# Kernel tuning notes

Measured on AMD Instinct MI355X. Metric: run time of the kernel, lower is better.

## Reference

```python
import jax, jax.numpy as jnp
import numpy as np

N = 50000
E = 800000
IN_C = 128
HID = 128
OUT_C = 2


def _linear_params(key, fan_in, fan_out):
    k1, k2 = jax.random.split(key)
    bound = 1.0 / np.sqrt(fan_in)
    W = jax.random.uniform(k1, (fan_in, fan_out), jnp.float32, -bound, bound)
    b = jax.random.uniform(k2, (fan_out,), jnp.float32, -bound, bound)
    return W, b


def setup_inputs() -> dict:
    key = jax.random.key(0)
    ks = jax.random.split(key, 9)
    x = jax.random.normal(ks[0], (N, IN_C), jnp.float32)
    edge_index = jax.random.randint(ks[1], (2, E), 0, N, jnp.int64)
    W1a, b1a = _linear_params(ks[2], IN_C, HID)
    W1b, b1b = _linear_params(ks[3], HID, HID)
    W2a, b2a = _linear_params(ks[4], HID, HID)
    W2b, b2b = _linear_params(ks[5], HID, HID)
    Wfc, bfc = _linear_params(ks[6], HID, OUT_C)
    return {
        "x": x, "edge_index": edge_index,
        "W1a": W1a, "b1a": b1a, "W1b": W1b, "b1b": b1b,
        "W2a": W2a, "b2a": b2a, "W2b": W2b, "b2b": b2b,
        "Wfc": Wfc, "bfc": bfc,
    }


def _gin_conv(x, src, dst, Wa, ba, Wb, bb):
    # GINConv with eps=0: h = MLP(x + sum_{j in N(i)} x_j)
    agg = jax.ops.segment_sum(x[src], dst, num_segments=N)  # [N, d]
    h = x + agg
    h = jax.nn.relu(h @ Wa + ba)
    return h @ Wb + bb


def reference(x, edge_index, W1a, b1a, W1b, b1b, W2a, b2a, W2b, b2b, Wfc, bfc):
    src, dst = edge_index[0], edge_index[1]  # messages flow src -> dst
    h = _gin_conv(x, src, dst, W1a, b1a, W1b, b1b)
    h = jax.nn.relu(h)
    # dropout is identity in eval mode
    h = _gin_conv(h, src, dst, W2a, b2a, W2b, b2b)
    return h @ Wfc + bfc  # [N, 2]
```

## Files before the change

### kernel.cpp

```cpp
#include <hip/hip_runtime.h>

#define N_NODES 50000
#define N_EDGES 800000
#define NBUK    392
#define B_BIN   128
#define EPB     6250
#define NCVT    1024
#define CAPB    2560

typedef unsigned short u16;
typedef unsigned int   u32;
typedef __bf16 bf16x8 __attribute__((ext_vector_type(8)));
typedef float  f32x4  __attribute__((ext_vector_type(4)));

__device__ __forceinline__ float bf_lo(u32 v){ return __uint_as_float(v << 16); }
__device__ __forceinline__ float bf_hi(u32 v){ return __uint_as_float(v & 0xffff0000u); }
__device__ __forceinline__ u32 bf_pack(float a, float b){
    u32 ua = __float_as_uint(a), ub = __float_as_uint(b);
    ua += 0x7fffu + ((ua >> 16) & 1u);
    ub += 0x7fffu + ((ub >> 16) & 1u);
    return (ua >> 16) | (ub & 0xffff0000u);
}
__device__ __forceinline__ u16 f2bf(float a){
    u32 ua = __float_as_uint(a);
    ua += 0x7fffu + ((ua >> 16) & 1u);
    return (u16)(ua >> 16);
}
__device__ __forceinline__ void addu4(uint4 v, float* a){
    a[0] += bf_lo(v.x); a[1] += bf_hi(v.x);
    a[2] += bf_lo(v.y); a[3] += bf_hi(v.y);
    a[4] += bf_lo(v.z); a[5] += bf_hi(v.z);
    a[6] += bf_lo(v.w); a[7] += bf_hi(v.w);
}

__device__ __forceinline__ int blockScan256(int v, int* ws, int t) {
    int lane = t & 63, w = t >> 6;
    #pragma unroll
    for (int off = 1; off < 64; off <<= 1) {
        int u = __shfl_up(v, off);
        if (lane >= off) v += u;
    }
    if (lane == 63) ws[w] = v;
    __syncthreads();
    int add = 0;
    for (int k = 0; k < w; k++) add += ws[k];
    return v + add;
}

__device__ __forceinline__ int blockScan512(int v, int* ws, int t) {
    int lane = t & 63, w = t >> 6;
    #pragma unroll
    for (int off = 1; off < 64; off <<= 1) {
        int u = __shfl_up(v, off);
        if (lane >= off) v += u;
    }
    if (lane == 63) ws[w] = v;
    __syncthreads();
    int add = 0;
    for (int k = 0; k < w; k++) add += ws[k];
    return v + add;
}

__launch_bounds__(256)
__global__ void binA_kernel(const int* __restrict__ esrc, const int* __restrict__ edst,
                            u32* __restrict__ bukBuf, int* __restrict__ bukCnt,
                            const float* __restrict__ xsrc, u32* __restrict__ xb,
                            const float* __restrict__ W1a, const float* __restrict__ W1b,
                            const float* __restrict__ W2a, const float* __restrict__ W2b,
                            const float* __restrict__ Wfc, const float* __restrict__ b2b,
                            const float* __restrict__ bfc,
                            u16* __restrict__ wt1a, u16* __restrict__ wt1b,
                            u16* __restrict__ wt2a,
                            float* __restrict__ Wc, float* __restrict__ bc) {
    int t = threadIdx.x, blk = blockIdx.x;
    __shared__ u32 ebuf[EPB];
    __shared__ int hist[NBUK];
    __shared__ int cur[NBUK];
    __shared__ int gbase[NBUK];
    __shared__ int ws[4];
    if (blk >= B_BIN) {
        int pb = blk - B_BIN;
        if (pb < 192) {
            int g  = pb * 256 + t;
            int mi = g >> 14;
            int p  = g & 16383;
            int k  = p >> 7, m = p & 127;
            const float* src = (mi == 0) ? W1a : (mi == 1) ? W1b : W2a;
            u16* dst         = (mi == 0) ? wt1a : (mi == 1) ? wt1b : wt2a;
            dst[m * 128 + k] = f2bf(src[k * 128 + m]);
            return;
        }
        if (pb == 192) {
            int j = t >> 1, o = t & 1;
            float s = 0.f;
            for (int k = 0; k < 128; k++)
                s += W2b[j * 128 + k] * Wfc[k * 2 + o];
            Wc[j * 2 + o] = s;
            if (t < 2) {
                float s2 = 0.f;
                for (int k = 0; k < 128; k++)
                    s2 += b2b[k] * Wfc[k * 2 + t];
                bc[t] = s2 + bfc[t];
            }
            return;
        }
        int cb = pb - 193;
        const int total = N_NODES * 64;
        for (int i = cb * 256 + t; i < total; i += NCVT * 256) {
            float2 f = ((const float2*)xsrc)[i];
            xb[i] = bf_pack(f.x, f.y);
        }
        return;
    }
    int base = blk * EPB;
    for (int i = t; i < NBUK; i += 256) hist[i] = 0;
    __syncthreads();
    for (int i = t; i < EPB; i += 256)
        atomicAdd(&hist[edst[base + i] >> 7], 1);
    __syncthreads();
    int c0 = 0, c1 = 0;
    if (t < 196) { c0 = hist[2 * t]; c1 = hist[2 * t + 1]; }
    int s2 = c0 + c1;
    int incl = blockScan256(s2, ws, t);
    int excl = incl - s2;
    if (t < 196) {
        hist[2 * t]     = excl;          cur[2 * t]     = excl;
        hist[2 * t + 1] = excl + c0;     cur[2 * t + 1] = excl + c0;
    }
    __syncthreads();
    for (int i = t; i < EPB; i += 256) {
        int gi = base + i;
        int d = edst[gi], s = esrc[gi];
        u32 e = (u32)s | ((u32)(d & 127) << 16) | ((u32)(d >> 7) << 23);
        int p = atomicAdd(&cur[d >> 7], 1);
        ebuf[p] = e;
    }
    __syncthreads();
    for (int j = t; j < NBUK; j += 256) {
        int cnt = cur[j] - hist[j];
        gbase[j] = cnt ? atomicAdd(&bukCnt[j], cnt) : 0;
    }
    __syncthreads();
    for (int i = t; i < EPB; i += 256) {
        u32 e = ebuf[i];
        int b9 = (int)(e >> 23);
        u32 idx = (u32)(gbase[b9] + (i - hist[b9]));
        if (idx < CAPB)
            bukBuf[(size_t)b9 * CAPB + idx] = e;
    }
}

__launch_bounds__(512, 4)
__global__ void bconv1_kernel(const u32* __restrict__ bukBuf,
                              const int* __restrict__ bukCnt,
                              const u32* __restrict__ xb,
                              const u16* __restrict__ WA, const float* __restrict__ bA,
                              const u16* __restrict__ WB, const float* __restrict__ bB,
                              int2* __restrict__ span, int* __restrict__ csr,
                              u16* __restrict__ h1, int n) {
    __shared__ __align__(16) char shbuf[34816 + 10240 + 512 + 512 + 32 + 16];
    u16 (*As)[136] = (u16(*)[136])shbuf;
    u32* ebuf      = (u32*)shbuf;
    int* cbuf      = (int*)(shbuf + 34816);
    int* hist      = (int*)(shbuf + 34816 + 10240);
    int* cursor    = (int*)(shbuf + 34816 + 10240 + 512);
    int* ws        = (int*)(shbuf + 34816 + 10240 + 1024);
    int b = blockIdx.x, t = threadIdx.x;

    int tot = bukCnt[b];
    if (tot > CAPB) tot = CAPB;
    if (t < 128) hist[t] = 0;
    __syncthreads();
    for (int i = t; i < tot; i += 512) {
        u32 e = bukBuf[(size_t)b * CAPB + i];
        ebuf[i] = e;
        atomicAdd(&hist[(e >> 16) & 127], 1);
    }
    __syncthreads();
    int hv = (t < 128) ? hist[t] : 0;
    int hincl = blockScan512(hv, ws, t);
    int hexcl = hincl - hv;
    int gb = b * CAPB;
    if (t < 128) {
        hist[t]   = hexcl;
        cursor[t] = hexcl;
        int node = (b << 7) + t;
        if (node < n) span[node] = make_int2(gb + hexcl, gb + hexcl + hv);
    }
    __syncthreads();
    for (int i = t; i < tot; i += 512) {
        u32 e = ebuf[i];
        int p = atomicAdd(&cursor[(e >> 16) & 127], 1);
        cbuf[p] = (int)(e & 0xFFFFu);
    }
    __syncthreads();
    for (int i = t; i < tot; i += 512)
        csr[gb + i] = cbuf[i];
    __syncthreads();

    int row0 = b * 128;
    int w = t >> 6, lane = t & 63;
    int g4 = lane >> 4, l16 = lane & 15;
    const uint4* xp = (const uint4*)xb;
    #pragma unroll
    for (int p = 0; p < 4; p++) {
        int rl = w * 16 + p * 4 + g4;
        int node = row0 + rl;
        float a[8] = {0.f,0.f,0.f,0.f,0.f,0.f,0.f,0.f};
        if (node < n) {
            addu4(xp[(size_t)node * 16 + l16], a);
            int j = hist[rl], jend = cursor[rl];
            for (; j + 8 <= jend; j += 8) {
                int s0 = cbuf[j],     s1 = cbuf[j + 1], s2b = cbuf[j + 2], s3 = cbuf[j + 3];
                int s4 = cbuf[j + 4], s5 = cbuf[j + 5], s6 = cbuf[j + 6], s7 = cbuf[j + 7];
                uint4 v0 = xp[(size_t)s0 * 16 + l16], v1 = xp[(size_t)s1 * 16 + l16];
                uint4 v2 = xp[(size_t)s2b * 16 + l16], v3 = xp[(size_t)s3 * 16 + l16];
                uint4 v4 = xp[(size_t)s4 * 16 + l16], v5 = xp[(size_t)s5 * 16 + l16];
                uint4 v6 = xp[(size_t)s6 * 16 + l16], v7 = xp[(size_t)s7 * 16 + l16];
                addu4(v0, a); addu4(v1, a); addu4(v2, a); addu4(v3, a);
                addu4(v4, a); addu4(v5, a); addu4(v6, a); addu4(v7, a);
            }
            for (; j + 4 <= jend; j += 4) {
                int s0 = cbuf[j], s1 = cbuf[j + 1], s2b = cbuf[j + 2], s3 = cbuf[j + 3];
                uint4 v0 = xp[(size_t)s0 * 16 + l16], v1 = xp[(size_t)s1 * 16 + l16];
                uint4 v2 = xp[(size_t)s2b * 16 + l16], v3 = xp[(size_t)s3 * 16 + l16];
                addu4(v0, a); addu4(v1, a); addu4(v2, a); addu4(v3, a);
            }
            for (; j < jend; j++)
                addu4(xp[(size_t)cbuf[j] * 16 + l16], a);
        }
        uint4 pk = make_uint4(bf_pack(a[0], a[1]), bf_pack(a[2], a[3]),
                              bf_pack(a[4], a[5]), bf_pack(a[6], a[7]));
        *(uint4*)&As[rl][l16 * 8] = pk;
    }
    int lm = l16, lq = g4;
    f32x4 acc[8];
    #pragma unroll
    for (int c = 0; c < 8; c++) acc[c] = (f32x4){0.f, 0.f, 0.f, 0.f};
    #pragma unroll
    for (int kk = 0; kk < 4; kk++) {
        bf16x8 af = *(const bf16x8*)&As[w * 16 + lm][kk * 32 + lq * 8];
        #pragma unroll
        for (int c = 0; c < 8; c++) {
            bf16x8 bf = *(const bf16x8*)(WA + (size_t)(c * 16 + lm) * 128 + kk * 32 + lq * 8);
            acc[c] = __builtin_amdgcn_mfma_f32_16x16x32_bf16(af, bf, acc[c], 0, 0, 0);
        }
    }
    #pragma unroll
    for (int c = 0; c < 8; c++) {
        int col = c * 16 + lm;
        float bcol = bA[col];
        #pragma unroll
        for (int r = 0; r < 4; r++) {
            float v = acc[c][r] + bcol;
            v = v > 0.f ? v : 0.f;
            As[w * 16 + lq * 4 + r][col] = f2bf(v);
        }
    }
    f32x4 acc2[8];
    #pragma unroll
    for (int c = 0; c < 8; c++) acc2[c] = (f32x4){0.f, 0.f, 0.f, 0.f};
    #pragma unroll
    for (int kk = 0; kk < 4; kk++) {
        bf16x8 af = *(const bf16x8*)&As[w * 16 + lm][kk * 32 + lq * 8];
        #pragma unroll
        for (int c = 0; c < 8; c++) {
            bf16x8 bf = *(const bf16x8*)(WB + (size_t)(c * 16 + lm) * 128 + kk * 32 + lq * 8);
            acc2[c] = __builtin_amdgcn_mfma_f32_16x16x32_bf16(af, bf, acc2[c], 0, 0, 0);
        }
    }
    #pragma unroll
    for (int c = 0; c < 8; c++) {
        int col = c * 16 + lm;
        float bcol = bB[col];
        #pragma unroll
        for (int r = 0; r < 4; r++) {
            int row = row0 + w * 16 + lq * 4 + r;
            if (row < n) {
                float v = acc2[c][r] + bcol;
                v = v > 0.f ? v : 0.f;
                h1[(size_t)row * 128 + col] = f2bf(v);
            }
        }
    }
}

__launch_bounds__(256, 4)
__global__ void fconv2_kernel(const u32* __restrict__ xb,
                              const u16* __restrict__ WA, const float* __restrict__ bA,
                              const float* __restrict__ Wc, const float* __restrict__ bc,
                              const int2* __restrict__ span, const int* __restrict__ csr,
                              float2* __restrict__ out, int n) {
    __shared__ u16 As[64][136];
    int t = threadIdx.x;
    int row0 = blockIdx.x * 64;
    int w = t >> 6, lane = t & 63;
    int g4 = lane >> 4, l16 = lane & 15;
    const uint4* xp = (const uint4*)xb;
    #pragma unroll
    for (int p = 0; p < 4; p++) {
        int rl = w * 16 + p * 4 + g4;
        int node = row0 + rl;
        float a[8] = {0.f,0.f,0.f,0.f,0.f,0.f,0.f,0.f};
        if (node < n) {
            addu4(xp[(size_t)node * 16 + l16], a);
            int2 sp = span[node];
            int j = sp.x, jend = sp.y;
            for (; j + 8 <= jend; j += 8) {
                int s0 = csr[j],     s1 = csr[j + 1], s2 = csr[j + 2], s3 = csr[j + 3];
                int s4 = csr[j + 4], s5 = csr[j + 5], s6 = csr[j + 6], s7 = csr[j + 7];
                uint4 v0 = xp[(size_t)s0 * 16 + l16], v1 = xp[(size_t)s1 * 16 + l16];
                uint4 v2 = xp[(size_t)s2 * 16 + l16], v3 = xp[(size_t)s3 * 16 + l16];
                uint4 v4 = xp[(size_t)s4 * 16 + l16], v5 = xp[(size_t)s5 * 16 + l16];
                uint4 v6 = xp[(size_t)s6 * 16 + l16], v7 = xp[(size_t)s7 * 16 + l16];
                addu4(v0, a); addu4(v1, a); addu4(v2, a); addu4(v3, a);
                addu4(v4, a); addu4(v5, a); addu4(v6, a); addu4(v7, a);
            }
            for (; j + 4 <= jend; j += 4) {
                int s0 = csr[j], s1 = csr[j + 1], s2 = csr[j + 2], s3 = csr[j + 3];
                uint4 v0 = xp[(size_t)s0 * 16 + l16], v1 = xp[(size_t)s1 * 16 + l16];
                uint4 v2 = xp[(size_t)s2 * 16 + l16], v3 = xp[(size_t)s3 * 16 + l16];
                addu4(v0, a); addu4(v1, a); addu4(v2, a); addu4(v3, a);
            }
            for (; j < jend; j++)
                addu4(xp[(size_t)csr[j] * 16 + l16], a);
        }
        uint4 pk = make_uint4(bf_pack(a[0], a[1]), bf_pack(a[2], a[3]),
                              bf_pack(a[4], a[5]), bf_pack(a[6], a[7]));
        *(uint4*)&As[rl][l16 * 8] = pk;
    }
    int lm = l16, lq = g4;
    f32x4 acc[8];
    #pragma unroll
    for (int c = 0; c < 8; c++) acc[c] = (f32x4){0.f, 0.f, 0.f, 0.f};
    #pragma unroll
    for (int kk = 0; kk < 4; kk++) {
        bf16x8 af = *(const bf16x8*)&As[w * 16 + lm][kk * 32 + lq * 8];
        #pragma unroll
        for (int c = 0; c < 8; c++) {
            bf16x8 bf = *(const bf16x8*)(WA + (size_t)(c * 16 + lm) * 128 + kk * 32 + lq * 8);
            acc[c] = __builtin_amdgcn_mfma_f32_16x16x32_bf16(af, bf, acc[c], 0, 0, 0);
        }
    }
    float p0[4] = {0,0,0,0}, p1[4] = {0,0,0,0};
    #pragma unroll
    for (int c = 0; c < 8; c++) {
        int col = c * 16 + lm;
        float bcol = bA[col];
        float2 wc = ((const float2*)Wc)[col];
        #pragma unroll
        for (int r = 0; r < 4; r++) {
            float v = acc[c][r] + bcol;
            v = v > 0.f ? v : 0.f;
            p0[r] += v * wc.x;
            p1[r] += v * wc.y;
        }
    }
    #pragma unroll
    for (int off = 1; off < 16; off <<= 1) {
        #pragma unroll
        for (int r = 0; r < 4; r++) {
            p0[r] += __shfl_xor(p0[r], off);
            p1[r] += __shfl_xor(p1[r], off);
        }
    }
    if (lm == 0) {
        float b0 = bc[0], b1 = bc[1];
        #pragma unroll
        for (int r = 0; r < 4; r++) {
            int row = row0 + w * 16 + lq * 4 + r;
            if (row < n) out[row] = make_float2(p0[r] + b0, p1[r] + b1);
        }
    }
}

extern "C" void kernel_launch(void* const* d_in, const int* in_sizes, int n_in,
                              void* d_out, int out_size, void* d_ws, size_t ws_size,
                              hipStream_t stream) {
    const float* x   = (const float*)d_in[0];
    const int*   ei  = (const int*)d_in[1];
    const float* W1a = (const float*)d_in[2];
    const float* b1a = (const float*)d_in[3];
    const float* W1b = (const float*)d_in[4];
    const float* b1b = (const float*)d_in[5];
    const float* W2a = (const float*)d_in[6];
    const float* b2a = (const float*)d_in[7];
    const float* W2b = (const float*)d_in[8];
    const float* b2b = (const float*)d_in[9];
    const float* Wfc = (const float*)d_in[10];
    const float* bfc = (const float*)d_in[11];

    const int* esrc = ei;
    const int* edst = ei + N_EDGES;

    char* w = (char*)d_ws;
    size_t off = 0;
    auto alloc = [&](size_t bytes) -> char* {
        char* p = w + off;
        off = (off + bytes + 255) & ~(size_t)255;
        return p;
    };
    int2*  span       = (int2*)alloc((size_t)N_NODES * 8);
    int*   csr        = (int*)alloc((size_t)NBUK * CAPB * 4);
    u32*   bukBuf     = (u32*)alloc((size_t)NBUK * CAPB * 4);
    int*   bukCnt     = (int*)alloc((size_t)NBUK * 4);
    u16*   wt1a       = (u16*)alloc(128 * 128 * 2);
    u16*   wt1b       = (u16*)alloc(128 * 128 * 2);
    u16*   wt2a       = (u16*)alloc(128 * 128 * 2);
    float* Wc         = (float*)alloc(256 * 4);
    float* bc         = (float*)alloc(2 * 4);
    u16*   bufA       = (u16*)alloc((size_t)N_NODES * 128 * 2);
    u16*   bufB       = (u16*)alloc((size_t)N_NODES * 128 * 2);

    hipMemsetAsync(bukCnt, 0, (size_t)NBUK * 4, stream);
    binA_kernel<<<B_BIN + 193 + NCVT, 256, 0, stream>>>(esrc, edst, bukBuf, bukCnt,
                                                        x, (u32*)bufB,
                                                        W1a, W1b, W2a, W2b, Wfc, b2b, bfc,
                                                        wt1a, wt1b, wt2a, Wc, bc);
    bconv1_kernel<<<NBUK, 512, 0, stream>>>(bukBuf, bukCnt,
                                            (const u32*)bufB, wt1a, b1a, wt1b, b1b,
                                            span, csr, bufA, N_NODES);
    fconv2_kernel<<<(N_NODES + 63) / 64, 256, 0, stream>>>((const u32*)bufA, wt2a, b2a,
                                                           Wc, bc, span, csr,
                                                           (float2*)d_out, N_NODES);
}
```

Measured before the change: 213.0 us.

## Split CSR build from conv1 and use persistent per-wave tile queues

Moves CSR construction out of the fused conv1 kernel into its own kernel. Both convolution kernels become persistent grids in which each wave independently takes 16-row tiles, first from a static per-block chunk and then from a global atomic counter. The aim is to even out the load imbalance caused by varying node degrees, which previously left whole 128-row blocks waiting at barriers. The cost is an extra kernel launch, a reread of csr from global memory instead of LDS in conv1, and atomic contention on the tile counters.

```diff
diff --git a/kernel.cpp b/kernel.cpp
--- a/kernel.cpp
+++ b/kernel.cpp
@@ -7,6 +7,10 @@
 #define EPB     6250
 #define NCVT    1024
 #define CAPB    2560
+#define NTILES  3125
+#define CGRID   768
+#define SCHUNK  3
+#define QBASE   (CGRID*SCHUNK)
 
 typedef unsigned short u16;
 typedef unsigned int   u32;
@@ -150,23 +154,15 @@
     }
 }
 
-__launch_bounds__(512, 4)
-__global__ void bconv1_kernel(const u32* __restrict__ bukBuf,
-                              const int* __restrict__ bukCnt,
-                              const u32* __restrict__ xb,
-                              const u16* __restrict__ WA, const float* __restrict__ bA,
-                              const u16* __restrict__ WB, const float* __restrict__ bB,
-                              int2* __restrict__ span, int* __restrict__ csr,
-                              u16* __restrict__ h1, int n) {
-    __shared__ __align__(16) char shbuf[34816 + 10240 + 512 + 512 + 32 + 16];
-    u16 (*As)[136] = (u16(*)[136])shbuf;
-    u32* ebuf      = (u32*)shbuf;
-    int* cbuf      = (int*)(shbuf + 34816);
-    int* hist      = (int*)(shbuf + 34816 + 10240);
-    int* cursor    = (int*)(shbuf + 34816 + 10240 + 512);
-    int* ws        = (int*)(shbuf + 34816 + 10240 + 1024);
+__launch_bounds__(512)
+__global__ void csrb_kernel(const u32* __restrict__ bukBuf, const int* __restrict__ bukCnt,
+                            int2* __restrict__ span, int* __restrict__ csr, int n) {
+    __shared__ u32 ebuf[CAPB];
+    __shared__ int cbuf[CAPB];
+    __shared__ int hist[128];
+    __shared__ int cursor[128];
+    __shared__ int ws[8];
     int b = blockIdx.x, t = threadIdx.x;
-
     int tot = bukCnt[b];
     if (tot > CAPB) tot = CAPB;
     if (t < 128) hist[t] = 0;
@@ -196,113 +192,37 @@
     __syncthreads();
     for (int i = t; i < tot; i += 512)
         csr[gb + i] = cbuf[i];
-    __syncthreads();
-
-    int row0 = b * 128;
+}
+
+__launch_bounds__(512, 4)
+__global__ void conv1q_kernel(const u32* __restrict__ xb,
+                              const u16* __restrict__ WA, const float* __restrict__ bA,
+                              const u16* __restrict__ WB, const float* __restrict__ bB,
+                              const int2* __restrict__ span, const int* __restrict__ csr,
+                              u16* __restrict__ h1, int* __restrict__ gctr) {
+    __shared__ __align__(16) u16 As[128][136];
+    __shared__ int lqc;
+    int t = threadIdx.x;
+    if (t == 0) lqc = 0;
+    __syncthreads();
     int w = t >> 6, lane = t & 63;
     int g4 = lane >> 4, l16 = lane & 15;
     const uint4* xp = (const uint4*)xb;
-    #pragma unroll
-    for (int p = 0; p < 4; p++) {
-        int rl = w * 16 + p * 4 + g4;
-        int node = row0 + rl;
-        float a[8] = {0.f,0.f,0.f,0.f,0.f,0.f,0.f,0.f};
-        if (node < n) {
-            addu4(xp[(size_t)node * 16 + l16], a);
-            int j = hist[rl], jend = cursor[rl];
-            for (; j + 8 <= jend; j += 8) {
-                int s0 = cbuf[j],     s1 = cbuf[j + 1], s2b = cbuf[j + 2], s3 = cbuf[j + 3];
-                int s4 = cbuf[j + 4], s5 = cbuf[j + 5], s6 = cbuf[j + 6], s7 = cbuf[j + 7];
-                uint4 v0 = xp[(size_t)s0 * 16 + l16], v1 = xp[(size_t)s1 * 16 + l16];
-                uint4 v2 = xp[(size_t)s2b * 16 + l16], v3 = xp[(size_t)s3 * 16 + l16];
-                uint4 v4 = xp[(size_t)s4 * 16 + l16], v5 = xp[(size_t)s5 * 16 + l16];
-                uint4 v6 = xp[(size_t)s6 * 16 + l16], v7 = xp[(size_t)s7 * 16 + l16];
-                addu4(v0, a); addu4(v1, a); addu4(v2, a); addu4(v3, a);
-                addu4(v4, a); addu4(v5, a); addu4(v6, a); addu4(v7, a);
-            }
-            for (; j + 4 <= jend; j += 4) {
-                int s0 = cbuf[j], s1 = cbuf[j + 1], s2b = cbuf[j + 2], s3 = cbuf[j + 3];
-                uint4 v0 = xp[(size_t)s0 * 16 + l16], v1 = xp[(size_t)s1 * 16 + l16];
-                uint4 v2 = xp[(size_t)s2b * 16 + l16], v3 = xp[(size_t)s3 * 16 + l16];
-                addu4(v0, a); addu4(v1, a); addu4(v2, a); addu4(v3, a);
-            }
-            for (; j < jend; j++)
-                addu4(xp[(size_t)cbuf[j] * 16 + l16], a);
-        }
-        uint4 pk = make_uint4(bf_pack(a[0], a[1]), bf_pack(a[2], a[3]),
-                              bf_pack(a[4], a[5]), bf_pack(a[6], a[7]));
-        *(uint4*)&As[rl][l16 * 8] = pk;
-    }
-    int lm = l16, lq = g4;
-    f32x4 acc[8];
-    #pragma unroll
-    for (int c = 0; c < 8; c++) acc[c] = (f32x4){0.f, 0.f, 0.f, 0.f};
-    #pragma unroll
-    for (int kk = 0; kk < 4; kk++) {
-        bf16x8 af = *(const bf16x8*)&As[w * 16 + lm][kk * 32 + lq * 8];
-        #pragma unroll
-        for (int c = 0; c < 8; c++) {
-            bf16x8 bf = *(const bf16x8*)(WA + (size_t)(c * 16 + lm) * 128 + kk * 32 + lq * 8);
-            acc[c] = __builtin_amdgcn_mfma_f32_16x16x32_bf16(af, bf, acc[c], 0, 0, 0);
-        }
-    }
-    #pragma unroll
-    for (int c = 0; c < 8; c++) {
-        int col = c * 16 + lm;
-        float bcol = bA[col];
-        #pragma unroll
-        for (int r = 0; r < 4; r++) {
-            float v = acc[c][r] + bcol;
-            v = v > 0.f ? v : 0.f;
-            As[w * 16 + lq * 4 + r][col] = f2bf(v);
-        }
-    }
-    f32x4 acc2[8];
-    #pragma unroll
-    for (int c = 0; c < 8; c++) acc2[c] = (f32x4){0.f, 0.f, 0.f, 0.f};
-    #pragma unroll
-    for (int kk = 0; kk < 4; kk++) {
-        bf16x8 af = *(const bf16x8*)&As[w * 16 + lm][kk * 32 + lq * 8];
-        #pragma unroll
-        for (int c = 0; c < 8; c++) {
-            bf16x8 bf = *(const bf16x8*)(WB + (size_t)(c * 16 + lm) * 128 + kk * 32 + lq * 8);
-            acc2[c] = __builtin_amdgcn_mfma_f32_16x16x32_bf16(af, bf, acc2[c], 0, 0, 0);
-        }
-    }
-    #pragma unroll
-    for (int c = 0; c < 8; c++) {
-        int col = c * 16 + lm;
-        float bcol = bB[col];
-        #pragma unroll
-        for (int r = 0; r < 4; r++) {
-            int row = row0 + w * 16 + lq * 4 + r;
-            if (row < n) {
-                float v = acc2[c][r] + bcol;
-                v = v > 0.f ? v : 0.f;
-                h1[(size_t)row * 128 + col] = f2bf(v);
-            }
-        }
-    }
-}
-
-__launch_bounds__(256, 4)
-__global__ void fconv2_kernel(const u32* __restrict__ xb,
-                              const u16* __restrict__ WA, const float* __restrict__ bA,
-                              const float* __restrict__ Wc, const float* __restrict__ bc,
-                              const int2* __restrict__ span, const int* __restrict__ csr,
-                              float2* __restrict__ out, int n) {
-    __shared__ u16 As[64][136];
-    int t = threadIdx.x;
-    int row0 = blockIdx.x * 64;
-    int w = t >> 6, lane = t & 63;
-    int g4 = lane >> 4, l16 = lane & 15;
-    const uint4* xp = (const uint4*)xb;
-    #pragma unroll
-    for (int p = 0; p < 4; p++) {
-        int rl = w * 16 + p * 4 + g4;
-        int node = row0 + rl;
-        float a[8] = {0.f,0.f,0.f,0.f,0.f,0.f,0.f,0.f};
-        if (node < n) {
+    int sbase = blockIdx.x * SCHUNK;
+    for (;;) {
+        int tk;
+        if (lane == 0) {
+            tk = atomicAdd(&lqc, 1);
+            tk = (tk < SCHUNK) ? (sbase + tk) : (QBASE + atomicAdd(gctr, 1));
+        }
+        tk = __shfl(tk, 0);
+        if (tk >= NTILES) break;
+        int row0 = tk << 4;
+        #pragma unroll
+        for (int p = 0; p < 4; p++) {
+            int rl = p * 4 + g4;
+            int node = row0 + rl;
+            float a[8] = {0.f,0.f,0.f,0.f,0.f,0.f,0.f,0.f};
             addu4(xp[(size_t)node * 16 + l16], a);
             int2 sp = span[node];
             int j = sp.x, jend = sp.y;
@@ -324,52 +244,155 @@
             }
             for (; j < jend; j++)
                 addu4(xp[(size_t)csr[j] * 16 + l16], a);
-        }
-        uint4 pk = make_uint4(bf_pack(a[0], a[1]), bf_pack(a[2], a[3]),
-                              bf_pack(a[4], a[5]), bf_pack(a[6], a[7]));
-        *(uint4*)&As[rl][l16 * 8] = pk;
-    }
-    int lm = l16, lq = g4;
-    f32x4 acc[8];
-    #pragma unroll
-    for (int c = 0; c < 8; c++) acc[c] = (f32x4){0.f, 0.f, 0.f, 0.f};
-    #pragma unroll
-    for (int kk = 0; kk < 4; kk++) {
-        bf16x8 af = *(const bf16x8*)&As[w * 16 + lm][kk * 32 + lq * 8];
+            uint4 pk = make_uint4(bf_pack(a[0], a[1]), bf_pack(a[2], a[3]),
+                                  bf_pack(a[4], a[5]), bf_pack(a[6], a[7]));
+            *(uint4*)&As[w * 16 + rl][l16 * 8] = pk;
+        }
+        f32x4 acc[8];
+        #pragma unroll
+        for (int c = 0; c < 8; c++) acc[c] = (f32x4){0.f, 0.f, 0.f, 0.f};
+        #pragma unroll
+        for (int kk = 0; kk < 4; kk++) {
+            bf16x8 af = *(const bf16x8*)&As[w * 16 + l16][kk * 32 + g4 * 8];
+            #pragma unroll
+            for (int c = 0; c < 8; c++) {
+                bf16x8 bf = *(const bf16x8*)(WA + (size_t)(c * 16 + l16) * 128 + kk * 32 + g4 * 8);
+                acc[c] = __builtin_amdgcn_mfma_f32_16x16x32_bf16(af, bf, acc[c], 0, 0, 0);
+            }
+        }
         #pragma unroll
         for (int c = 0; c < 8; c++) {
-            bf16x8 bf = *(const bf16x8*)(WA + (size_t)(c * 16 + lm) * 128 + kk * 32 + lq * 8);
-            acc[c] = __builtin_amdgcn_mfma_f32_16x16x32_bf16(af, bf, acc[c], 0, 0, 0);
-        }
-    }
-    float p0[4] = {0,0,0,0}, p1[4] = {0,0,0,0};
-    #pragma unroll
-    for (int c = 0; c < 8; c++) {
-        int col = c * 16 + lm;
-        float bcol = bA[col];
-        float2 wc = ((const float2*)Wc)[col];
-        #pragma unroll
-        for (int r = 0; r < 4; r++) {
-            float v = acc[c][r] + bcol;
-            v = v > 0.f ? v : 0.f;
-            p0[r] += v * wc.x;
-            p1[r] += v * wc.y;
-        }
-    }
-    #pragma unroll
-    for (int off = 1; off < 16; off <<= 1) {
-        #pragma unroll
-        for (int r = 0; r < 4; r++) {
-            p0[r] += __shfl_xor(p0[r], off);
-            p1[r] += __shfl_xor(p1[r], off);
-        }
-    }
-    if (lm == 0) {
-        float b0 = bc[0], b1 = bc[1];
-        #pragma unroll
-        for (int r = 0; r < 4; r++) {
-            int row = row0 + w * 16 + lq * 4 + r;
-            if (row < n) out[row] = make_float2(p0[r] + b0, p1[r] + b1);
+            int col = c * 16 + l16;
+            float bcol = bA[col];
+            #pragma unroll
+            for (int r = 0; r < 4; r++) {
+                float v = acc[c][r] + bcol;
+                v = v > 0.f ? v : 0.f;
+                As[w * 16 + g4 * 4 + r][col] = f2bf(v);
+            }
+        }
+        f32x4 acc2[8];
+        #pragma unroll
+        for (int c = 0; c < 8; c++) acc2[c] = (f32x4){0.f, 0.f, 0.f, 0.f};
+        #pragma unroll
+        for (int kk = 0; kk < 4; kk++) {
+            bf16x8 af = *(const bf16x8*)&As[w * 16 + l16][kk * 32 + g4 * 8];
+            #pragma unroll
+            for (int c = 0; c < 8; c++) {
+                bf16x8 bf = *(const bf16x8*)(WB + (size_t)(c * 16 + l16) * 128 + kk * 32 + g4 * 8);
+                acc2[c] = __builtin_amdgcn_mfma_f32_16x16x32_bf16(af, bf, acc2[c], 0, 0, 0);
+            }
+        }
+        #pragma unroll
+        for (int c = 0; c < 8; c++) {
+            int col = c * 16 + l16;
+            float bcol = bB[col];
+            #pragma unroll
+            for (int r = 0; r < 4; r++) {
+                int row = row0 + g4 * 4 + r;
+                float v = acc2[c][r] + bcol;
+                v = v > 0.f ? v : 0.f;
+                h1[(size_t)row * 128 + col] = f2bf(v);
+            }
+        }
+    }
+}
+
+__launch_bounds__(512, 4)
+__global__ void conv2q_kernel(const u32* __restrict__ xb,
+                              const u16* __restrict__ WA, const float* __restrict__ bA,
+                              const float* __restrict__ Wc, const float* __restrict__ bc,
+                              const int2* __restrict__ span, const int* __restrict__ csr,
+                              float2* __restrict__ out, int* __restrict__ gctr) {
+    __shared__ __align__(16) u16 As[128][136];
+    __shared__ int lqc;
+    int t = threadIdx.x;
+    if (t == 0) lqc = 0;
+    __syncthreads();
+    int w = t >> 6, lane = t & 63;
+    int g4 = lane >> 4, l16 = lane & 15;
+    const uint4* xp = (const uint4*)xb;
+    int sbase = blockIdx.x * SCHUNK;
+    float b0 = bc[0], b1 = bc[1];
+    for (;;) {
+        int tk;
+        if (lane == 0) {
+            tk = atomicAdd(&lqc, 1);
+            tk = (tk < SCHUNK) ? (sbase + tk) : (QBASE + atomicAdd(gctr, 1));
+        }
+        tk = __shfl(tk, 0);
+        if (tk >= NTILES) break;
+        int row0 = tk << 4;
+        #pragma unroll
+        for (int p = 0; p < 4; p++) {
+            int rl = p * 4 + g4;
+            int node = row0 + rl;
+            float a[8] = {0.f,0.f,0.f,0.f,0.f,0.f,0.f,0.f};
+            addu4(xp[(size_t)node * 16 + l16], a);
+            int2 sp = span[node];
+            int j = sp.x, jend = sp.y;
+            for (; j + 8 <= jend; j += 8) {
+                int s0 = csr[j],     s1 = csr[j + 1], s2 = csr[j + 2], s3 = csr[j + 3];
+                int s4 = csr[j + 4], s5 = csr[j + 5], s6 = csr[j + 6], s7 = csr[j + 7];
+                uint4 v0 = xp[(size_t)s0 * 16 + l16], v1 = xp[(size_t)s1 * 16 + l16];
+                uint4 v2 = xp[(size_t)s2 * 16 + l16], v3 = xp[(size_t)s3 * 16 + l16];
+                uint4 v4 = xp[(size_t)s4 * 16 + l16], v5 = xp[(size_t)s5 * 16 + l16];
+                uint4 v6 = xp[(size_t)s6 * 16 + l16], v7 = xp[(size_t)s7 * 16 + l16];
+                addu4(v0, a); addu4(v1, a); addu4(v2, a); addu4(v3, a);
+                addu4(v4, a); addu4(v5, a); addu4(v6, a); addu4(v7, a);
+            }
+            for (; j + 4 <= jend; j += 4) {
+                int s0 = csr[j], s1 = csr[j + 1], s2 = csr[j + 2], s3 = csr[j + 3];
+                uint4 v0 = xp[(size_t)s0 * 16 + l16], v1 = xp[(size_t)s1 * 16 + l16];
+                uint4 v2 = xp[(size_t)s2 * 16 + l16], v3 = xp[(size_t)s3 * 16 + l16];
+                addu4(v0, a); addu4(v1, a); addu4(v2, a); addu4(v3, a);
+            }
+            for (; j < jend; j++)
+                addu4(xp[(size_t)csr[j] * 16 + l16], a);
+            uint4 pk = make_uint4(bf_pack(a[0], a[1]), bf_pack(a[2], a[3]),
+                                  bf_pack(a[4], a[5]), bf_pack(a[6], a[7]));
+            *(uint4*)&As[w * 16 + rl][l16 * 8] = pk;
+        }
+        f32x4 acc[8];
+        #pragma unroll
+        for (int c = 0; c < 8; c++) acc[c] = (f32x4){0.f, 0.f, 0.f, 0.f};
+        #pragma unroll
+        for (int kk = 0; kk < 4; kk++) {
+            bf16x8 af = *(const bf16x8*)&As[w * 16 + l16][kk * 32 + g4 * 8];
+            #pragma unroll
+            for (int c = 0; c < 8; c++) {
+                bf16x8 bf = *(const bf16x8*)(WA + (size_t)(c * 16 + l16) * 128 + kk * 32 + g4 * 8);
+                acc[c] = __builtin_amdgcn_mfma_f32_16x16x32_bf16(af, bf, acc[c], 0, 0, 0);
+            }
+        }
+        float p0[4] = {0,0,0,0}, p1[4] = {0,0,0,0};
+        #pragma unroll
+        for (int c = 0; c < 8; c++) {
+            int col = c * 16 + l16;
+            float bcol = bA[col];
+            float2 wc = ((const float2*)Wc)[col];
+            #pragma unroll
+            for (int r = 0; r < 4; r++) {
+                float v = acc[c][r] + bcol;
+                v = v > 0.f ? v : 0.f;
+                p0[r] += v * wc.x;
+                p1[r] += v * wc.y;
+            }
+        }
+        #pragma unroll
+        for (int off = 1; off < 16; off <<= 1) {
+            #pragma unroll
+            for (int r = 0; r < 4; r++) {
+                p0[r] += __shfl_xor(p0[r], off);
+                p1[r] += __shfl_xor(p1[r], off);
+            }
+        }
+        if (l16 == 0) {
+            #pragma unroll
+            for (int r = 0; r < 4; r++) {
+                int row = row0 + g4 * 4 + r;
+                out[row] = make_float2(p0[r] + b0, p1[r] + b1);
+            }
         }
     }
 }
@@ -403,7 +426,7 @@
     int2*  span       = (int2*)alloc((size_t)N_NODES * 8);
     int*   csr        = (int*)alloc((size_t)NBUK * CAPB * 4);
     u32*   bukBuf     = (u32*)alloc((size_t)NBUK * CAPB * 4);
-    int*   bukCnt     = (int*)alloc((size_t)NBUK * 4);
+    int*   meta       = (int*)alloc((size_t)(NBUK + 8) * 4);
     u16*   wt1a       = (u16*)alloc(128 * 128 * 2);
     u16*   wt1b       = (u16*)alloc(128 * 128 * 2);
     u16*   wt2a       = (u16*)alloc(128 * 128 * 2);
@@ -412,15 +435,18 @@
     u16*   bufA       = (u16*)alloc((size_t)N_NODES * 128 * 2);
     u16*   bufB       = (u16*)alloc((size_t)N_NODES * 128 * 2);
 
-    hipMemsetAsync(bukCnt, 0, (size_t)NBUK * 4, stream);
+    int* bukCnt = meta;
+    int* gc1    = meta + NBUK;
+    int* gc2    = meta + NBUK + 1;
+
+    hipMemsetAsync(meta, 0, (size_t)(NBUK + 8) * 4, stream);
     binA_kernel<<<B_BIN + 193 + NCVT, 256, 0, stream>>>(esrc, edst, bukBuf, bukCnt,
                                                         x, (u32*)bufB,
                                                         W1a, W1b, W2a, W2b, Wfc, b2b, bfc,
                                                         wt1a, wt1b, wt2a, Wc, bc);
-    bconv1_kernel<<<NBUK, 512, 0, stream>>>(bukBuf, bukCnt,
-                                            (const u32*)bufB, wt1a, b1a, wt1b, b1b,
-                                            span, csr, bufA, N_NODES);
-    fconv2_kernel<<<(N_NODES + 63) / 64, 256, 0, stream>>>((const u32*)bufA, wt2a, b2a,
-                                                           Wc, bc, span, csr,
-                                                           (float2*)d_out, N_NODES);
-}
+    csrb_kernel<<<NBUK, 512, 0, stream>>>(bukBuf, bukCnt, span, csr, N_NODES);
+    conv1q_kernel<<<CGRID, 512, 0, stream>>>((const u32*)bufB, wt1a, b1a, wt1b, b1b,
+                                             span, csr, bufA, gc1);
+    conv2q_kernel<<<CGRID, 512, 0, stream>>>((const u32*)bufA, wt2a, b2a, Wc, bc,
+                                             span, csr, (float2*)d_out, gc2);
+}
```

New measurement: 392.4 us. +84.2%, slower.
